# Kernel optimization log

Measured on AMD Instinct MI355X. Metric: run time of the kernel, lower is better.

The kernel has to match this reference:

```python
import jax, jax.numpy as jnp
import numpy as np

B, S, D, H = 2, 2048, 1024, 16
DK = D // H
THETA = 10000.0


def _freqs_cos_sin(dim, seq_len, theta=THETA):
    # matches precompute_freqs_cis: freqs over full d_model, pairs of adjacent dims
    inv = 1.0 / theta ** (np.arange(0, dim, 2)[: dim // 2].astype(np.float32) / dim)
    t = np.arange(seq_len, dtype=np.float32)
    ang = np.outer(t, inv)  # [S, D/2]
    return jnp.asarray(np.cos(ang)), jnp.asarray(np.sin(ang))


def setup_inputs() -> dict:
    key = jax.random.key(0)
    ks = jax.random.split(key, 11)
    sc = 1.0 / np.sqrt(D)
    cos, sin = _freqs_cos_sin(D, S)
    return {
        "query": jax.random.normal(ks[0], (B, S, D), jnp.float32),
        "key": jax.random.normal(ks[1], (B, S, D), jnp.float32),
        "value": jax.random.normal(ks[2], (B, S, D), jnp.float32),
        "wq": jax.random.normal(ks[3], (D, D), jnp.float32) * sc,
        "bq": jnp.zeros((D,), jnp.float32),
        "wk": jax.random.normal(ks[4], (D, D), jnp.float32) * sc,
        "bk": jnp.zeros((D,), jnp.float32),
        "wv": jax.random.normal(ks[5], (D, D), jnp.float32) * sc,
        "bv": jnp.zeros((D,), jnp.float32),
        "wo": jax.random.normal(ks[6], (D, D), jnp.float32) * sc,
        "bo": jnp.zeros((D,), jnp.float32),
        "cos": cos,  # [S, D/2]
        "sin": sin,  # [S, D/2]
    }


def _rope(x, cos, sin):
    # x: [B,S,D]; pairs are adjacent elements along D (view_as_complex semantics)
    xr = x.reshape(*x.shape[:-1], -1, 2)  # [B,S,D/2,2]
    x0, x1 = xr[..., 0], xr[..., 1]
    c, s = cos[None], sin[None]  # broadcast over batch
    o0 = x0 * c - x1 * s
    o1 = x0 * s + x1 * c
    return jnp.stack([o0, o1], axis=-1).reshape(x.shape)


def reference(query, key, value, wq, bq, wk, bk, wv, bv, wo, bo, cos, sin):
    q = query @ wq.T + bq
    k = key @ wk.T + bk
    v = value @ wv.T + bv
    q = _rope(q, cos, sin)
    k = _rope(k, cos, sin)
    # split heads: [B,S,D] -> [B,H,S,DK]
    q = q.reshape(B, S, H, DK).transpose(0, 2, 1, 3)
    k = k.reshape(B, S, H, DK).transpose(0, 2, 1, 3)
    v = v.reshape(B, S, H, DK).transpose(0, 2, 1, 3)
    scores = jnp.einsum("bhqd,bhkd->bhqk", q, k) / jnp.sqrt(jnp.float32(DK))
    attn = jax.nn.softmax(scores, axis=-1)  # dropout is identity in eval
    out = jnp.einsum("bhqk,bhkd->bhqd", attn, v)
    out = out.transpose(0, 2, 1, 3).reshape(B, S, D)
    return out @ wo.T + bo
```

## Files before the change

kernel.cpp:

```cpp
#include <hip/hip_runtime.h>
#include <hip/hip_fp16.h>

typedef _Float16 f16;
using f16x8 = __attribute__((ext_vector_type(8))) _Float16;
using h2 = __attribute__((ext_vector_type(2))) __fp16;
using f32x4 = __attribute__((ext_vector_type(4))) float;
using f32x16 = __attribute__((ext_vector_type(16))) float;

#define LOG2E 1.4426950408889634f

__device__ __forceinline__ void gload16(const void* g, void* l) {
  __builtin_amdgcn_global_load_lds(
      (const __attribute__((address_space(1))) void*)g,
      (__attribute__((address_space(3))) void*)l, 16, 0, 0);
}

__device__ __forceinline__ float b32(h2 x) { return __builtin_bit_cast(float, x); }
__device__ __forceinline__ unsigned u32(h2 x) { return __builtin_bit_cast(unsigned, x); }

__global__ __launch_bounds__(256) void convert_k(
    const float* __restrict__ q, const float* __restrict__ k, const float* __restrict__ v,
    const float* __restrict__ wq, const float* __restrict__ wk,
    const float* __restrict__ wv, const float* __restrict__ wo,
    f16* __restrict__ dst) {
  const size_t SEG = (size_t)4 * 1024 * 1024;
  size_t i = ((size_t)blockIdx.x * 256 + threadIdx.x) * 8;
  const float* src; size_t off;
  if (i < SEG)            { src = q;  off = i; }
  else if (i < 2 * SEG)   { src = k;  off = i - SEG; }
  else if (i < 3 * SEG)   { src = v;  off = i - 2 * SEG; }
  else {
    size_t wi = i - 3 * SEG;
    int s = (int)(wi >> 20);
    src = (s == 0) ? wq : (s == 1) ? wk : (s == 2) ? wv : wo;
    off = wi & ((1u << 20) - 1);
  }
  float4 a = *(const float4*)(src + off);
  float4 b = *(const float4*)(src + off + 4);
  f16x8 o;
  o[0] = (f16)a.x; o[1] = (f16)a.y; o[2] = (f16)a.z; o[3] = (f16)a.w;
  o[4] = (f16)b.x; o[5] = (f16)b.y; o[6] = (f16)b.z; o[7] = (f16)b.w;
  *(f16x8*)(dst + i) = o;
}

template <int QKV>
__global__ __launch_bounds__(256) void gemm_k(
    const f16* __restrict__ Abase, const f16* __restrict__ Wbase,
    const float* __restrict__ b0, const float* __restrict__ b1, const float* __restrict__ b2,
    const float* __restrict__ cosT, const float* __restrict__ sinT,
    f16* __restrict__ qh, f16* __restrict__ kh, f16* __restrict__ vt,
    float* __restrict__ outF) {
  __shared__ f16 As[128 * 32];
  __shared__ f16 Bs[128 * 32];
  int tid = threadIdx.x, wid = tid >> 6, lane = tid & 63;
  int z = QKV ? blockIdx.z : 0;
  const f16* A = Abase + (size_t)z * (4u * 1024 * 1024);
  const f16* W = Wbase + (size_t)z * (1024u * 1024);
  int m0 = blockIdx.y * 128, n0 = blockIdx.x * 128;
  int wr = wid >> 1, wc = wid & 1;
  f32x4 acc[4][4] = {};

  for (int kt = 0; kt < 32; ++kt) {
    int k0 = kt * 32;
    __syncthreads();
#pragma unroll
    for (int p = 0; p < 2; ++p) {
      int row = p * 64 + (tid >> 2);
      int srcslot = (tid & 3) ^ (row & 3);
      gload16(A + (size_t)(m0 + row) * 1024 + k0 + srcslot * 8,
              (void*)(As + p * 2048 + wid * 512));
      gload16(W + (size_t)(n0 + row) * 1024 + k0 + srcslot * 8,
              (void*)(Bs + p * 2048 + wid * 512));
    }
    __syncthreads();
    f16x8 af[4], bf[4];
#pragma unroll
    for (int i = 0; i < 4; ++i) {
      int row = wr * 64 + i * 16 + (lane & 15);
      int slot = (lane >> 4) ^ (row & 3);
      af[i] = *(const f16x8*)(As + row * 32 + slot * 8);
    }
#pragma unroll
    for (int j = 0; j < 4; ++j) {
      int col = wc * 64 + j * 16 + (lane & 15);
      int slot = (lane >> 4) ^ (col & 3);
      bf[j] = *(const f16x8*)(Bs + col * 32 + slot * 8);
    }
#pragma unroll
    for (int i = 0; i < 4; ++i)
#pragma unroll
      for (int j = 0; j < 4; ++j)
        acc[i][j] = __builtin_amdgcn_mfma_f32_16x16x32_f16(af[i], bf[j], acc[i][j], 0, 0, 0);
  }

  const float* bias = QKV ? (z == 0 ? b0 : (z == 1 ? b1 : b2)) : b0;
#pragma unroll
  for (int i = 0; i < 4; ++i) {
#pragma unroll
    for (int j = 0; j < 4; ++j) {
#pragma unroll
      for (int r = 0; r < 4; ++r) {
        int grow = m0 + wr * 64 + i * 16 + ((lane >> 4) << 2) + r;
        int gcol = n0 + wc * 64 + j * 16 + (lane & 15);
        float val = acc[i][j][r] + bias[gcol];
        if (QKV) {
          int s = grow & 2047, bb = grow >> 11;
          int h = gcol >> 6, dk = gcol & 63;
          if (z < 2) {
            float pr = __shfl_xor(val, 1);
            int j2 = gcol >> 1;
            float c = cosT[s * 512 + j2], sn = sinT[s * 512 + j2];
            val = (lane & 1) ? (c * val + sn * pr) : (c * val - sn * pr);
            if (z == 0) val *= 0.125f * LOG2E;
            f16* dst = (z == 0) ? qh : kh;
            dst[(((size_t)bb * 16 + h) * 2048 + s) * 64 + dk] = (f16)val;
          } else {
            vt[(((size_t)bb * 16 + h) * 64 + dk) * 2048 + s] = (f16)val;
          }
        } else {
          outF[(size_t)grow * 1024 + gcol] = val;
        }
      }
    }
  }
}

__global__ __launch_bounds__(128) void flash_k(
    const f16* __restrict__ qh, const f16* __restrict__ kh, const f16* __restrict__ vt,
    f16* __restrict__ attnout) {
  __shared__ f16 Ks[2][64 * 64];
  __shared__ f16 Vs[2][64 * 64];
  int tid = threadIdx.x, wid = tid >> 6, lane = tid & 63;
  int l31 = lane & 31, hi = lane >> 5;
  int qt = blockIdx.x, h = blockIdx.y, bz = blockIdx.z;
  size_t bh = (size_t)bz * 16 + h;
  const f16* qp = qh + bh * (2048 * 64);
  const f16* kp = kh + bh * (2048 * 64);
  const f16* vp = vt + bh * (64 * 2048);
  int qrow = qt * 64 + wid * 32 + l31;

  f16x8 qf[4];
#pragma unroll
  for (int kk = 0; kk < 4; ++kk)
    qf[kk] = *(const f16x8*)(qp + (size_t)qrow * 64 + kk * 16 + hi * 8);

  int srow = tid >> 3;
  int sch = (tid & 7) ^ (srow & 7);
  const f16* ksrc = kp + (size_t)srow * 64 + sch * 8;
  const f16* vsrc = vp + (size_t)srow * 2048 + sch * 8;

  int offr[2][4];
#pragma unroll
  for (int kb = 0; kb < 2; ++kb)
#pragma unroll
    for (int kk = 0; kk < 4; ++kk) {
      int row = kb * 32 + l31;
      offr[kb][kk] = (row * 128 + kk * 32 + hi * 16) ^ ((row & 7) << 4);
    }

  float m_ = -1e30f, l_ = 0.f;
  f32x16 oacc[2] = {};

#pragma unroll
  for (int p = 0; p < 4; ++p) {
    gload16(ksrc + (size_t)p * (16 * 64), (char*)&Ks[0][0] + (p * 128 + tid) * 16);
    gload16(vsrc + (size_t)p * (16 * 2048), (char*)&Vs[0][0] + (p * 128 + tid) * 16);
  }
  __syncthreads();

  int cur = 0;
  for (int kt = 0; kt < 32; ++kt) {
    if (kt + 1 < 32) {
#pragma unroll
      for (int p = 0; p < 4; ++p) {
        gload16(ksrc + (size_t)(kt + 1) * 4096 + (size_t)p * (16 * 64),
                (char*)&Ks[cur ^ 1][0] + (p * 128 + tid) * 16);
        gload16(vsrc + (size_t)(kt + 1) * 64 + (size_t)p * (16 * 2048),
                (char*)&Vs[cur ^ 1][0] + (p * 128 + tid) * 16);
      }
    }

    const char* kbase = (const char*)&Ks[cur][0];
    f32x16 sacc[2] = {};
#pragma unroll
    for (int kb = 0; kb < 2; ++kb)
#pragma unroll
      for (int kk = 0; kk < 4; ++kk) {
        f16x8 af = *(const f16x8*)(kbase + offr[kb][kk]);
        sacc[kb] = __builtin_amdgcn_mfma_f32_32x32x16_f16(af, qf[kk], sacc[kb], 0, 0, 0);
      }

    float pmax = -1e30f;
#pragma unroll
    for (int kb = 0; kb < 2; ++kb)
#pragma unroll
      for (int i = 0; i < 16; ++i) pmax = fmaxf(pmax, sacc[kb][i]);
    pmax = fmaxf(pmax, __shfl_xor(pmax, 32));
    float mn = fmaxf(m_, pmax);
    float al = __builtin_amdgcn_exp2f(m_ - mn);
    m_ = mn;
    float rs = 0.f;
#pragma unroll
    for (int kb = 0; kb < 2; ++kb)
#pragma unroll
      for (int i = 0; i < 16; ++i) {
        float pv = __builtin_amdgcn_exp2f(sacc[kb][i] - mn);
        sacc[kb][i] = pv; rs += pv;
      }
    rs += __shfl_xor(rs, 32);
    l_ = l_ * al + rs;
#pragma unroll
    for (int mb = 0; mb < 2; ++mb)
#pragma unroll
      for (int i = 0; i < 16; ++i) oacc[mb][i] *= al;

    f16x8 pa[4];
#pragma unroll
    for (int kk = 0; kk < 4; ++kk) {
      int kb = kk >> 1, c8 = (kk & 1) * 8;
      float wA = b32(__builtin_amdgcn_cvt_pkrtz(sacc[kb][c8 + 0], sacc[kb][c8 + 1]));
      float wB = b32(__builtin_amdgcn_cvt_pkrtz(sacc[kb][c8 + 2], sacc[kb][c8 + 3]));
      float wC = b32(__builtin_amdgcn_cvt_pkrtz(sacc[kb][c8 + 4], sacc[kb][c8 + 5]));
      float wD = b32(__builtin_amdgcn_cvt_pkrtz(sacc[kb][c8 + 6], sacc[kb][c8 + 7]));
      float oA = __shfl_xor(wA, 32), oB = __shfl_xor(wB, 32);
      float oC = __shfl_xor(wC, 32), oD = __shfl_xor(wD, 32);
      float4 ff;
      ff.x = hi ? oC : wA;
      ff.y = hi ? oD : wB;
      ff.z = hi ? wC : oA;
      ff.w = hi ? wD : oB;
      pa[kk] = __builtin_bit_cast(f16x8, ff);
    }

    const char* vbase = (const char*)&Vs[cur][0];
#pragma unroll
    for (int kk = 0; kk < 4; ++kk)
#pragma unroll
      for (int mb = 0; mb < 2; ++mb) {
        f16x8 av = *(const f16x8*)(vbase + offr[mb][kk]);
        oacc[mb] = __builtin_amdgcn_mfma_f32_32x32x16_f16(av, pa[kk], oacc[mb], 0, 0, 0);
      }

    __syncthreads();
    cur ^= 1;
  }

  float inv = 1.f / l_;
  f16* orow = attnout + ((size_t)bz * 2048 + qrow) * 1024 + h * 64;
#pragma unroll
  for (int mb = 0; mb < 2; ++mb)
#pragma unroll
    for (int g = 0; g < 4; ++g) {
      uint2 st;
      st.x = u32(__builtin_amdgcn_cvt_pkrtz(oacc[mb][4 * g + 0] * inv, oacc[mb][4 * g + 1] * inv));
      st.y = u32(__builtin_amdgcn_cvt_pkrtz(oacc[mb][4 * g + 2] * inv, oacc[mb][4 * g + 3] * inv));
      *(uint2*)(orow + mb * 32 + g * 8 + hi * 4) = st;
    }
}

extern "C" void kernel_launch(void* const* d_in, const int* in_sizes, int n_in,
                              void* d_out, int out_size, void* d_ws, size_t ws_size,
                              hipStream_t stream) {
  (void)in_sizes; (void)n_in; (void)out_size; (void)ws_size;
  const float* query = (const float*)d_in[0];
  const float* key   = (const float*)d_in[1];
  const float* value = (const float*)d_in[2];
  const float* wq = (const float*)d_in[3];
  const float* bq = (const float*)d_in[4];
  const float* wk = (const float*)d_in[5];
  const float* bk = (const float*)d_in[6];
  const float* wv = (const float*)d_in[7];
  const float* bv = (const float*)d_in[8];
  const float* wo = (const float*)d_in[9];
  const float* bo = (const float*)d_in[10];
  const float* cosT = (const float*)d_in[11];
  const float* sinT = (const float*)d_in[12];
  float* out = (float*)d_out;
  f16* ws = (f16*)d_ws;
  const size_t SEG = (size_t)4 * 1024 * 1024;
  f16* Xh = ws;
  f16* Wh = ws + 3 * SEG;
  f16* qh = ws + 16u * 1024 * 1024;
  f16* kh = qh + SEG;
  f16* vt = kh + SEG;
  f16* attnout = ws;

  convert_k<<<8192, 256, 0, stream>>>(query, key, value, wq, wk, wv, wo, ws);
  gemm_k<1><<<dim3(8, 32, 3), 256, 0, stream>>>(Xh, Wh, bq, bk, bv, cosT, sinT,
                                                qh, kh, vt, nullptr);
  flash_k<<<dim3(32, 16, 2), 128, 0, stream>>>(qh, kh, vt, attnout);
  gemm_k<0><<<dim3(8, 32, 1), 256, 0, stream>>>(attnout, Wh + 3u * 1024 * 1024, bo,
                                                nullptr, nullptr, nullptr, nullptr,
                                                nullptr, nullptr, nullptr, out);
}
```

Before: 173.0 us.

## Split attention over two key halves with a combine kernel, dropping LDS staging

The flash kernel now splits the key sequence into two halves (split-K), with each block handling 128 query rows across four waves and reading K/V fragments straight from global memory instead of double-buffered LDS. It also skips the running-max rescale unless the new max exceeds the old one by a threshold, and uses tree reductions for max and sum. A new combine kernel merges the two partial outputs using the stored (m, l) pairs. The aim is to remove LDS traffic and barriers and to raise parallelism, at the cost of extra global reads per wave, partial-output writes and an additional launch.

```diff
diff --git a/kernel.cpp b/kernel.cpp
--- a/kernel.cpp
+++ b/kernel.cpp
@@ -125,94 +125,72 @@
   }
 }
 
-__global__ __launch_bounds__(128) void flash_k(
+__global__ __launch_bounds__(256, 4) void flash_k(
     const f16* __restrict__ qh, const f16* __restrict__ kh, const f16* __restrict__ vt,
-    f16* __restrict__ attnout) {
-  __shared__ f16 Ks[2][64 * 64];
-  __shared__ f16 Vs[2][64 * 64];
+    f16* __restrict__ op, float2* __restrict__ mlbuf) {
   int tid = threadIdx.x, wid = tid >> 6, lane = tid & 63;
   int l31 = lane & 31, hi = lane >> 5;
-  int qt = blockIdx.x, h = blockIdx.y, bz = blockIdx.z;
-  size_t bh = (size_t)bz * 16 + h;
+  int qt = blockIdx.x, h = blockIdx.y, z = blockIdx.z;
+  int b = z >> 1, ks = z & 1;
+  size_t bh = (size_t)b * 16 + h;
   const f16* qp = qh + bh * (2048 * 64);
   const f16* kp = kh + bh * (2048 * 64);
   const f16* vp = vt + bh * (64 * 2048);
-  int qrow = qt * 64 + wid * 32 + l31;
+  int qrow = qt * 128 + wid * 32 + l31;
 
   f16x8 qf[4];
 #pragma unroll
   for (int kk = 0; kk < 4; ++kk)
     qf[kk] = *(const f16x8*)(qp + (size_t)qrow * 64 + kk * 16 + hi * 8);
 
-  int srow = tid >> 3;
-  int sch = (tid & 7) ^ (srow & 7);
-  const f16* ksrc = kp + (size_t)srow * 64 + sch * 8;
-  const f16* vsrc = vp + (size_t)srow * 2048 + sch * 8;
-
-  int offr[2][4];
-#pragma unroll
-  for (int kb = 0; kb < 2; ++kb)
-#pragma unroll
-    for (int kk = 0; kk < 4; ++kk) {
-      int row = kb * 32 + l31;
-      offr[kb][kk] = (row * 128 + kk * 32 + hi * 16) ^ ((row & 7) << 4);
-    }
+  const f16* kbp = kp + ((size_t)ks * 1024 + l31) * 64 + hi * 8;
+  const f16* vbp = vp + (size_t)l31 * 2048 + ks * 1024 + hi * 8;
 
   float m_ = -1e30f, l_ = 0.f;
   f32x16 oacc[2] = {};
 
-#pragma unroll
-  for (int p = 0; p < 4; ++p) {
-    gload16(ksrc + (size_t)p * (16 * 64), (char*)&Ks[0][0] + (p * 128 + tid) * 16);
-    gload16(vsrc + (size_t)p * (16 * 2048), (char*)&Vs[0][0] + (p * 128 + tid) * 16);
-  }
-  __syncthreads();
-
-  int cur = 0;
-  for (int kt = 0; kt < 32; ++kt) {
-    if (kt + 1 < 32) {
-#pragma unroll
-      for (int p = 0; p < 4; ++p) {
-        gload16(ksrc + (size_t)(kt + 1) * 4096 + (size_t)p * (16 * 64),
-                (char*)&Ks[cur ^ 1][0] + (p * 128 + tid) * 16);
-        gload16(vsrc + (size_t)(kt + 1) * 64 + (size_t)p * (16 * 2048),
-                (char*)&Vs[cur ^ 1][0] + (p * 128 + tid) * 16);
-      }
-    }
-
-    const char* kbase = (const char*)&Ks[cur][0];
+  for (int kt = 0; kt < 16; ++kt) {
     f32x16 sacc[2] = {};
 #pragma unroll
     for (int kb = 0; kb < 2; ++kb)
 #pragma unroll
       for (int kk = 0; kk < 4; ++kk) {
-        f16x8 af = *(const f16x8*)(kbase + offr[kb][kk]);
+        f16x8 af = *(const f16x8*)(kbp + (size_t)(kt * 64 + kb * 32) * 64 + kk * 16);
         sacc[kb] = __builtin_amdgcn_mfma_f32_32x32x16_f16(af, qf[kk], sacc[kb], 0, 0, 0);
       }
 
-    float pmax = -1e30f;
+    float t16[16];
+#pragma unroll
+    for (int i = 0; i < 16; ++i) t16[i] = fmaxf(sacc[0][i], sacc[1][i]);
+#pragma unroll
+    for (int s = 8; s; s >>= 1)
+#pragma unroll
+      for (int i = 0; i < s; ++i) t16[i] = fmaxf(t16[i], t16[i + s]);
+    float pmax = fmaxf(t16[0], __shfl_xor(t16[0], 32));
+
+    if (!__all(pmax <= m_ + 8.0f)) {
+      float mn = fmaxf(m_, pmax);
+      float al = __builtin_amdgcn_exp2f(m_ - mn);
+      m_ = mn;
+      l_ *= al;
+#pragma unroll
+      for (int mb = 0; mb < 2; ++mb)
+#pragma unroll
+        for (int i = 0; i < 16; ++i) oacc[mb][i] *= al;
+    }
+
 #pragma unroll
     for (int kb = 0; kb < 2; ++kb)
 #pragma unroll
-      for (int i = 0; i < 16; ++i) pmax = fmaxf(pmax, sacc[kb][i]);
-    pmax = fmaxf(pmax, __shfl_xor(pmax, 32));
-    float mn = fmaxf(m_, pmax);
-    float al = __builtin_amdgcn_exp2f(m_ - mn);
-    m_ = mn;
-    float rs = 0.f;
-#pragma unroll
-    for (int kb = 0; kb < 2; ++kb)
-#pragma unroll
-      for (int i = 0; i < 16; ++i) {
-        float pv = __builtin_amdgcn_exp2f(sacc[kb][i] - mn);
-        sacc[kb][i] = pv; rs += pv;
-      }
-    rs += __shfl_xor(rs, 32);
-    l_ = l_ * al + rs;
-#pragma unroll
-    for (int mb = 0; mb < 2; ++mb)
-#pragma unroll
-      for (int i = 0; i < 16; ++i) oacc[mb][i] *= al;
+      for (int i = 0; i < 16; ++i)
+        sacc[kb][i] = __builtin_amdgcn_exp2f(sacc[kb][i] - m_);
+#pragma unroll
+    for (int i = 0; i < 16; ++i) t16[i] = sacc[0][i] + sacc[1][i];
+#pragma unroll
+    for (int s = 8; s; s >>= 1)
+#pragma unroll
+      for (int i = 0; i < s; ++i) t16[i] += t16[i + s];
+    l_ += t16[0] + __shfl_xor(t16[0], 32);
 
     f16x8 pa[4];
 #pragma unroll
@@ -232,21 +210,17 @@
       pa[kk] = __builtin_bit_cast(f16x8, ff);
     }
 
-    const char* vbase = (const char*)&Vs[cur][0];
 #pragma unroll
     for (int kk = 0; kk < 4; ++kk)
 #pragma unroll
       for (int mb = 0; mb < 2; ++mb) {
-        f16x8 av = *(const f16x8*)(vbase + offr[mb][kk]);
+        f16x8 av = *(const f16x8*)(vbp + (size_t)(mb * 32) * 2048 + kt * 64 + kk * 16);
         oacc[mb] = __builtin_amdgcn_mfma_f32_32x32x16_f16(av, pa[kk], oacc[mb], 0, 0, 0);
       }
-
-    __syncthreads();
-    cur ^= 1;
   }
 
   float inv = 1.f / l_;
-  f16* orow = attnout + ((size_t)bz * 2048 + qrow) * 1024 + h * 64;
+  f16* orow = op + (((size_t)z * 16 + h) * 2048 + qrow) * 64;
 #pragma unroll
   for (int mb = 0; mb < 2; ++mb)
 #pragma unroll
@@ -256,6 +230,30 @@
       st.y = u32(__builtin_amdgcn_cvt_pkrtz(oacc[mb][4 * g + 2] * inv, oacc[mb][4 * g + 3] * inv));
       *(uint2*)(orow + mb * 32 + g * 8 + hi * 4) = st;
     }
+  if (hi == 0)
+    mlbuf[((size_t)z * 16 + h) * 2048 + qrow] = make_float2(m_, l_);
+}
+
+__global__ __launch_bounds__(256) void combine_k(
+    const f16* __restrict__ op, const float2* __restrict__ ml, f16* __restrict__ attnout) {
+  int t = blockIdx.x * 256 + threadIdx.x;
+  int row = t >> 3, c8 = t & 7;
+  int b = row >> 15, h = (row >> 11) & 15, qrow = row & 2047;
+  size_t i0 = ((size_t)(b * 2 + 0) * 16 + h) * 2048 + qrow;
+  size_t i1 = ((size_t)(b * 2 + 1) * 16 + h) * 2048 + qrow;
+  float2 a = ml[i0], c = ml[i1];
+  float M = fmaxf(a.x, c.x);
+  float w1 = a.y * __builtin_amdgcn_exp2f(a.x - M);
+  float w2 = c.y * __builtin_amdgcn_exp2f(c.x - M);
+  float inv = 1.f / (w1 + w2);
+  w1 *= inv; w2 *= inv;
+  f16x8 o1 = *(const f16x8*)(op + i0 * 64 + c8 * 8);
+  f16x8 o2 = *(const f16x8*)(op + i1 * 64 + c8 * 8);
+  f16x8 o;
+#pragma unroll
+  for (int e = 0; e < 8; ++e)
+    o[e] = (f16)(w1 * (float)o1[e] + w2 * (float)o2[e]);
+  *(f16x8*)(attnout + ((size_t)b * 2048 + qrow) * 1024 + h * 64 + c8 * 8) = o;
 }
 
 extern "C" void kernel_launch(void* const* d_in, const int* in_sizes, int n_in,
@@ -284,11 +282,14 @@
   f16* kh = qh + SEG;
   f16* vt = kh + SEG;
   f16* attnout = ws;
+  f16* op = ws + SEG;
+  float2* mlb = (float2*)(ws + 12u * 1024 * 1024);
 
   convert_k<<<8192, 256, 0, stream>>>(query, key, value, wq, wk, wv, wo, ws);
   gemm_k<1><<<dim3(8, 32, 3), 256, 0, stream>>>(Xh, Wh, bq, bk, bv, cosT, sinT,
                                                 qh, kh, vt, nullptr);
-  flash_k<<<dim3(32, 16, 2), 128, 0, stream>>>(qh, kh, vt, attnout);
+  flash_k<<<dim3(16, 16, 4), 256, 0, stream>>>(qh, kh, vt, op, mlb);
+  combine_k<<<2048, 256, 0, stream>>>(op, mlb, attnout);
   gemm_k<0><<<dim3(8, 32, 1), 256, 0, stream>>>(attnout, Wh + 3u * 1024 * 1024, bo,
                                                 nullptr, nullptr, nullptr, nullptr,
                                                 nullptr, nullptr, nullptr, out);
```

Measured after the change: 225.1 us. +30.1%, slower.
